# Optimization experiments

Hardware: AMD Instinct MI355X
Metric: run time of the kernel (lower is better)

## Reference

```python
import jax, jax.numpy as jnp
import numpy as np

# static sizes (see shape_source)
IN_SIZE = 50000
M = 3            # n_modalities
N0 = 40960       # layer-0 sampled source nodes
N1 = 16384       # layer-0 dst == layer-1 src
B = 4096         # batch (final dst nodes)
HEADS = 4
DIM = 64
HD = HEADS * DIM # 256, integration_size
DEG0, DEG1 = 16, 16
E0, E1 = N1 * DEG0, B * DEG1
NEG_SLOPE = 0.2  # GATConv default negative_slope


def gat_conv(x_src, e_src, e_dst, n_dst, W, att, bias):
    """PyG GATConv with bipartite input (x, None): attention uses only alpha_l.
    x_src: [Ns, HD]; W: [HD, HD]; att: [1, H, C]; returns [n_dst, HD]."""
    x_l = (x_src @ W.T).reshape(-1, HEADS, DIM)            # [Ns, H, C]
    alpha_l = (x_l * att).sum(-1)                          # [Ns, H]
    logits = jax.nn.leaky_relu(alpha_l[e_src], NEG_SLOPE)  # [E, H]
    m = jax.ops.segment_max(logits, e_dst, num_segments=n_dst)
    m = jnp.where(jnp.isfinite(m), m, 0.0)                 # guard empty segments
    e = jnp.exp(logits - m[e_dst])
    denom = jax.ops.segment_sum(e, e_dst, num_segments=n_dst)
    a = e / (denom[e_dst] + 1e-16)                         # edge softmax per dst
    msg = x_l[e_src] * a[:, :, None]                       # [E, H, C]
    out = jax.ops.segment_sum(msg, e_dst, num_segments=n_dst)
    return out.reshape(n_dst, HD) + bias


def interp(scales_param, mask, key):
    """Interp module, evaluate=False, idxs = range(M)."""
    scales = jax.nn.softmax(scales_param, axis=-1)         # [1, M]
    rm = jax.random.randint(key, mask.shape, 0, 2).astype(jnp.float32)
    rm = rm + (1.0 / (1.0 + rm.sum(-1)) ** 20)[:, None]
    rm = rm + (1.0 / (mask.sum(-1) ** 20))[:, None]
    rm = jax.lax.stop_gradient(jnp.floor(rm))              # .int().float()
    rm = rm / (rm + 1e-10)
    m = mask * rm
    m = jax.nn.softmax(m + (1.0 - m) * (-1e10), axis=-1)   # [B, M]
    return scales, m


def setup_inputs() -> dict:
    key = jax.random.key(0)
    ks = jax.random.split(key, 12)
    s = 0.05
    return {
        "masks": jnp.ones((B, M), jnp.float32),
        "n_ids": jax.random.randint(ks[0], (M, N0), 0, IN_SIZE, dtype=jnp.int32),
        "e0_src": jax.random.randint(ks[1], (M, E0), 0, N0, dtype=jnp.int32),
        "e0_dst": jnp.repeat(jnp.arange(N1, dtype=jnp.int32), DEG0),
        "e1_src": jax.random.randint(ks[2], (M, E1), 0, N1, dtype=jnp.int32),
        "e1_dst": jnp.repeat(jnp.arange(B, dtype=jnp.int32), DEG1),
        "pre_W": jax.random.normal(ks[3], (M, HD, IN_SIZE), jnp.float32) * s,
        "pre_b": jax.random.normal(ks[4], (M, HD), jnp.float32) * s,
        "gat_W": jax.random.normal(ks[5], (M, HD, HD), jnp.float32) * s,
        "gat_att": jax.random.normal(ks[6], (M, 1, HEADS, DIM), jnp.float32) * s,
        "gat_b": jax.random.normal(ks[7], (M, HD), jnp.float32) * s,
        "scales_param": jnp.full((1, M), 1.0 / M, jnp.float32),
        "emb_W": jax.random.normal(ks[8], (128, HD), jnp.float32) * s,
        "emb_b": jax.random.normal(ks[9], (128,), jnp.float32) * s,
    }


def reference(masks, n_ids, e0_src, e0_dst, e1_src, e1_dst,
              pre_W, pre_b, gat_W, gat_att, gat_b,
              scales_param, emb_W, emb_b):
    scales, interp_masks = interp(scales_param, masks, jax.random.key(42))
    x_mod = jnp.zeros((B, HD), dtype=masks.dtype)
    for i in range(M):  # small fixed modality loop (structurally distinct params)
        # one-hot(n_id) @ W.T + b  ==  gather of columns of W (same math)
        x = jnp.take(pre_W[i], n_ids[i], axis=1).T + pre_b[i]        # [N0, HD]
        g0 = gat_conv(x, e0_src[i], e0_dst, N1, gat_W[i], gat_att[i], gat_b[i])
        g1 = gat_conv(g0, e1_src[i], e1_dst, B, gat_W[i], gat_att[i], gat_b[i])
        # x_store_layer = [g0[:B] (sliced), g0[:B] (x_pre), g1]; x = sum + g1
        xm = 2.0 * g0[:B] + 2.0 * g1                                  # [B, HD]
        xm = scales[:, i] * interp_masks[:, i].reshape(-1, 1) * xm
        x_mod = x_mod + xm
    emb = x_mod @ emb_W.T + emb_b                                     # [B, 128]
    dot = emb @ emb.T                                                 # [B, B]
    return dot, emb, scales
```

## Files before the change

kernel.cpp:

```cpp
#include <hip/hip_runtime.h>
#include <hip/hip_bf16.h>
#include <cstdint>

#define IN_SZ 50000
#define NM 3
#define N0 40960
#define N1 16384
#define NB 4096
#define HD 256
#define DEG 16
#define E0 (N1*DEG)
#define E1 (NB*DEG)

using short8v = __attribute__((ext_vector_type(8))) short;
using floatx4 = __attribute__((ext_vector_type(4))) float;
typedef unsigned short ushort_t;

__device__ __forceinline__ ushort_t f2bf(float f){
  uint32_t u = __float_as_uint(f);
  uint32_t r = u + 0x7FFFu + ((u>>16)&1u);
  return (ushort_t)(r>>16);
}
__device__ __forceinline__ float bf2f(ushort_t h){
  return __uint_as_float(((uint32_t)h)<<16);
}
__device__ __forceinline__ void gload_lds16(const ushort_t* g, ushort_t* l){
  __builtin_amdgcn_global_load_lds(
      (const __attribute__((address_space(1))) void*)g,
      (__attribute__((address_space(3))) void*)l, 16, 0, 0);
}

__device__ __forceinline__ uint32_t rotl32(uint32_t x, uint32_t d){ return (x<<d)|(x>>(32u-d)); }

__device__ void tf2x32(uint32_t k0, uint32_t k1, uint32_t c0, uint32_t c1,
                       uint32_t& y0, uint32_t& y1)
{
  uint32_t ks2 = k0 ^ k1 ^ 0x1BD11BDAu;
  uint32_t x0 = c0 + k0, x1 = c1 + k1;
#define R4(a,b,c,d) \
  x0+=x1; x1=rotl32(x1,a); x1^=x0; \
  x0+=x1; x1=rotl32(x1,b); x1^=x0; \
  x0+=x1; x1=rotl32(x1,c); x1^=x0; \
  x0+=x1; x1=rotl32(x1,d); x1^=x0;
  R4(13,15,26,6)  x0+=k1;  x1+=ks2+1u;
  R4(17,29,16,24) x0+=ks2; x1+=k0+2u;
  R4(13,15,26,6)  x0+=k0;  x1+=k1+3u;
  R4(17,29,16,24) x0+=k1;  x1+=ks2+4u;
  R4(13,15,26,6)  x0+=ks2; x1+=k0+5u;
#undef R4
  y0=x0; y1=x1;
}

__global__ void interp_coef_k(const float* __restrict__ masks, const float* __restrict__ sp,
                              float* __restrict__ coef, float* __restrict__ scales_out)
{
  int b = blockIdx.x*256 + threadIdx.x;
  if (b >= NB) return;
  float s0=sp[0], s1=sp[1], s2=sp[2];
  float mx = fmaxf(s0,fmaxf(s1,s2));
  float e0=expf(s0-mx), e1=expf(s1-mx), e2=expf(s2-mx);
  float inv = 1.f/(e0+e1+e2);
  float sc[3] = {e0*inv, e1*inv, e2*inv};
  if (b == 0){ scales_out[0]=sc[0]; scales_out[1]=sc[1]; scales_out[2]=sc[2]; }

  uint32_t bits[3];
  uint32_t K0,K1, t0,t1;
  tf2x32(0u,42u,0u,1u,K0,K1);
  for (int i=0;i<3;i++){
    uint32_t idx = (uint32_t)(b*3+i);
    tf2x32(K0,K1,0u,idx,t0,t1);
    bits[i] = (t0 ^ t1) & 1u;
  }
  float mk[3] = {masks[b*3+0], masks[b*3+1], masks[b*3+2]};
  float msum = mk[0]+mk[1]+mk[2];
  float rs = (float)(bits[0]+bits[1]+bits[2]);
  float add = powf(1.f/(1.f+rs), 20.f) + powf(1.f/msum, 20.f);
  float lg[3]; float lmax = -1e30f;
  for (int i=0;i<3;i++){
    float rm = floorf((float)bits[i] + add);
    rm = rm/(rm+1e-10f);
    float mm = mk[i]*rm;
    lg[i] = mm + (1.f-mm)*(-1e10f);
    lmax = fmaxf(lmax, lg[i]);
  }
  float es[3], ssum=0.f;
  for (int i=0;i<3;i++){ es[i]=expf(lg[i]-lmax); ssum+=es[i]; }
  for (int i=0;i<3;i++) coef[b*3+i] = sc[i]*es[i]/ssum;
}

__global__ __launch_bounds__(256) void transp_k(const float* __restrict__ Wb,
                                                ushort_t* __restrict__ WT_b)
{
  int i = blockIdx.z;
  const float* W = Wb + (size_t)i*HD*IN_SZ;
  ushort_t* WT = WT_b + (size_t)i*IN_SZ*HD;
  __shared__ float tile[32][33];
  int c0 = blockIdx.x*32, k0 = blockIdx.y*32;
  int tx = threadIdx.x & 31, tg = threadIdx.x >> 5;
#pragma unroll
  for (int j=0;j<4;j++){
    int k = k0 + tg*4 + j, c = c0 + tx;
    tile[tg*4+j][tx] = (c < IN_SZ) ? W[(size_t)k*IN_SZ + c] : 0.f;
  }
  __syncthreads();
#pragma unroll
  for (int j=0;j<4;j++){
    int c = c0 + tg*4 + j, k = k0 + tx;
    if (c < IN_SZ) WT[(size_t)c*HD + k] = f2bf(tile[tx][tg*4+j]);
  }
}

__global__ void split_k(const float* __restrict__ src, ushort_t* __restrict__ hi,
                        ushort_t* __restrict__ lo, int n)
{
  int g = blockIdx.x*256 + threadIdx.x;
  if (g >= n) return;
  float v = src[g];
  ushort_t h = f2bf(v);
  hi[g] = h;
  lo[g] = f2bf(v - bf2f(h));
}

__global__ void bias_gemv_k(const float* __restrict__ pre_b, const float* __restrict__ gat_W,
                            float* __restrict__ bias2)
{
  int i = blockIdx.x, o = threadIdx.x;
  const float* W = gat_W + (size_t)i*HD*HD + (size_t)o*HD;
  const float* b = pre_b + i*HD;
  float s = 0.f;
  for (int k=0;k<HD;k++) s = fmaf(b[k], W[k], s);
  bias2[i*HD + o] = s;
}

template<bool HAS_IDS, bool ADD_BIAS>
__global__ __launch_bounds__(256) void gemm2(
    const ushort_t* __restrict__ A_b, size_t a_stride,
    const int* __restrict__ ids_b, int ids_n,
    const ushort_t* __restrict__ Whi_b, const ushort_t* __restrict__ Wlo_b,
    const float* __restrict__ bias2_b,
    ushort_t* __restrict__ C_b, size_t c_stride,
    const float* __restrict__ att_b, float* __restrict__ alpha_b, size_t al_stride)
{
  int i = blockIdx.z;
  int bn0 = blockIdx.y * 128;
  int brow = blockIdx.x * 128;
  const ushort_t* A = A_b + (size_t)i*a_stride;
  const ushort_t* Whi = Whi_b + (size_t)i*HD*HD;
  const ushort_t* Wlo = Wlo_b + (size_t)i*HD*HD;
  ushort_t* C = C_b + (size_t)i*c_stride;
  const float* att = att_b + (size_t)i*HD;
  float* alpha = alpha_b + (size_t)i*al_stride;

  __shared__ __align__(16) ushort_t smem[2][24*512];
  __shared__ int sid[128];
  int t = threadIdx.x, wave = t>>6, lane = t&63;
  int l15 = lane&15, kq = lane>>4;

  if constexpr (HAS_IDS){
    if (t < 128) sid[t] = ids_b[(size_t)i*ids_n + brow + t];
    __syncthreads();
  }
  int row0, row1;
  if constexpr (HAS_IDS){ row0 = sid[wave*16 + l15]; row1 = sid[(wave+4)*16 + l15]; }
  else                  { row0 = brow + wave*16 + l15; row1 = brow + (wave+4)*16 + l15; }

  const ushort_t* gsrc[6];
  gsrc[0] = A + (size_t)row0*HD + kq*8;
  gsrc[1] = A + (size_t)row1*HD + kq*8;
#pragma unroll
  for (int j=2;j<6;j++){
    int idx = wave + 4*(j-2);
    int ct = idx>>1, h = idx&1;
    const ushort_t* W = h ? Wlo : Whi;
    gsrc[j] = W + (size_t)(bn0 + ct*16 + l15)*HD + kq*8;
  }

  floatx4 acc[4][4];
#pragma unroll
  for (int r=0;r<4;r++)
#pragma unroll
    for (int c=0;c<4;c++) acc[r][c] = (floatx4){0.f,0.f,0.f,0.f};

  int wm = wave>>1, wn = wave&1;

#pragma unroll
  for (int j=0;j<6;j++)
    gload_lds16(gsrc[j], &smem[0][(wave + 4*j)*512]);
  __syncthreads();

  for (int cc=0; cc<8; cc++){
    int buf = cc & 1;
    if (cc < 7){
      int k0 = (cc+1)*32;
#pragma unroll
      for (int j=0;j<6;j++)
        gload_lds16(gsrc[j] + k0, &smem[buf^1][(wave + 4*j)*512]);
    }
    short8v a[4];
#pragma unroll
    for (int r=0;r<4;r++)
      a[r] = *reinterpret_cast<const short8v*>(&smem[buf][(wm*4+r)*512 + lane*8]);
#pragma unroll
    for (int c=0;c<4;c++){
      int ct = wn*4+c;
      short8v bh = *reinterpret_cast<const short8v*>(&smem[buf][(8+ct*2)*512 + lane*8]);
      short8v bl = *reinterpret_cast<const short8v*>(&smem[buf][(9+ct*2)*512 + lane*8]);
#pragma unroll
      for (int r=0;r<4;r++){
        acc[r][c] = __builtin_amdgcn_mfma_f32_16x16x32_bf16(a[r], bh, acc[r][c], 0,0,0);
        acc[r][c] = __builtin_amdgcn_mfma_f32_16x16x32_bf16(a[r], bl, acc[r][c], 0,0,0);
      }
    }
    __syncthreads();
  }

  float attv[4], bias2v[4];
#pragma unroll
  for (int c=0;c<4;c++){
    int col = bn0 + (wn*4+c)*16 + l15;
    attv[c] = att[col];
    if constexpr (ADD_BIAS) bias2v[c] = bias2_b[i*HD + col];
  }
  int head = (bn0>>6) + wn;
#pragma unroll
  for (int r=0;r<4;r++){
    int rowb = brow + wm*64 + r*16 + kq*4;
    if constexpr (ADD_BIAS){
#pragma unroll
      for (int c=0;c<4;c++)
#pragma unroll
        for (int j=0;j<4;j++) acc[r][c][j] += bias2v[c];
    }
#pragma unroll
    for (int j=0;j<4;j++){
      size_t rw = (size_t)(rowb + j)*HD;
#pragma unroll
      for (int c=0;c<4;c++)
        C[rw + bn0 + (wn*4+c)*16 + l15] = f2bf(acc[r][c][j]);
    }
#pragma unroll
    for (int j=0;j<4;j++){
      float p = acc[r][0][j]*attv[0] + acc[r][1][j]*attv[1]
              + acc[r][2][j]*attv[2] + acc[r][3][j]*attv[3];
      p += __shfl_xor(p, 1, 64);
      p += __shfl_xor(p, 2, 64);
      p += __shfl_xor(p, 4, 64);
      p += __shfl_xor(p, 8, 64);
      if (l15 == 0){
        float lg = p > 0.f ? p : 0.2f*p;
        alpha[(size_t)(rowb + j)*4 + head] = lg;
      }
    }
  }
}

__global__ __launch_bounds__(128) void gat_msg0(
    const ushort_t* __restrict__ xlhi_b, const float* __restrict__ alpha_b,
    const int* __restrict__ esrc_b, const float* __restrict__ bias_b,
    uint32_t* __restrict__ g0_u)
{
  int i = blockIdx.y, d = blockIdx.x, t = threadIdx.x;
  const ushort_t* xl = xlhi_b + (size_t)i*N0*HD;
  const float* alpha = alpha_b + (size_t)i*N0*4;
  const float* bias = bias_b + i*HD;
  __shared__ int src[16];
  __shared__ float aw[16][4];
  if (t < 16) src[t] = esrc_b[(size_t)i*E0 + d*16 + t];
  __syncthreads();
  if (t < 64){
    int e = t&15, h = t>>4;
    float l = alpha[(size_t)src[e]*4 + h];
    float m = l;
#pragma unroll
    for (int off=1; off<16; off<<=1) m = fmaxf(m, __shfl_xor(m, off, 64));
    float ex = expf(l - m);
    float s = ex;
#pragma unroll
    for (int off=1; off<16; off<<=1) s += __shfl_xor(s, off, 64);
    aw[e][h] = ex / (s + 1e-16f);
  }
  __syncthreads();
  int h = t >> 5;
  float a0=0.f, a1=0.f;
#pragma unroll
  for (int e=0;e<16;e++){
    uint32_t u = *reinterpret_cast<const uint32_t*>(xl + (size_t)src[e]*HD + 2*t);
    float w = aw[e][h];
    a0 = fmaf(w, bf2f((ushort_t)(u & 0xffffu)), a0);
    a1 = fmaf(w, bf2f((ushort_t)(u >> 16)), a1);
  }
  float v0 = a0 + bias[2*t], v1 = a1 + bias[2*t+1];
  g0_u[((size_t)i*N1 + d)*128 + t] = (uint32_t)f2bf(v0) | ((uint32_t)f2bf(v1)<<16);
}

__global__ __launch_bounds__(128) void gat_msg1(
    const ushort_t* __restrict__ xl1hi, const float* __restrict__ alpha1,
    const int* __restrict__ e1src, const float* __restrict__ gat_b,
    const uint32_t* __restrict__ g0_u, const float* __restrict__ coef,
    float* __restrict__ xmod)
{
  int d = blockIdx.x, t = threadIdx.x;
  __shared__ int src[16];
  __shared__ float aw[16][4];
  float o0 = 0.f, o1 = 0.f;
  for (int i=0;i<NM;i++){
    if (t < 16) src[t] = e1src[(size_t)i*E1 + d*16 + t];
    __syncthreads();
    if (t < 64){
      int e = t&15, h = t>>4;
      float l = alpha1[((size_t)i*N1 + src[e])*4 + h];
      float m = l;
#pragma unroll
      for (int off=1; off<16; off<<=1) m = fmaxf(m, __shfl_xor(m, off, 64));
      float ex = expf(l - m);
      float s = ex;
#pragma unroll
      for (int off=1; off<16; off<<=1) s += __shfl_xor(s, off, 64);
      aw[e][h] = ex / (s + 1e-16f);
    }
    __syncthreads();
    const ushort_t* xl = xl1hi + (size_t)i*N1*HD;
    int h = t >> 5;
    float a0=0.f, a1=0.f;
#pragma unroll
    for (int e=0;e<16;e++){
      uint32_t u = *reinterpret_cast<const uint32_t*>(xl + (size_t)src[e]*HD + 2*t);
      float w = aw[e][h];
      a0 = fmaf(w, bf2f((ushort_t)(u & 0xffffu)), a0);
      a1 = fmaf(w, bf2f((ushort_t)(u >> 16)), a1);
    }
    uint32_t gh = g0_u[((size_t)i*N1 + d)*128 + t];
    float g00 = bf2f((ushort_t)(gh & 0xffffu));
    float g01 = bf2f((ushort_t)(gh >> 16));
    const float* bias = gat_b + i*HD;
    float cv = coef[d*3 + i];
    o0 += cv*(2.f*g00 + 2.f*(a0 + bias[2*t]));
    o1 += cv*(2.f*g01 + 2.f*(a1 + bias[2*t+1]));
    __syncthreads();
  }
  *reinterpret_cast<float2*>(&xmod[(size_t)d*HD + 2*t]) = make_float2(o0, o1);
}

__global__ void transp_embW(const float* __restrict__ w, float* __restrict__ wt)
{
  int g = blockIdx.x*256 + threadIdx.x;
  int j = g >> 8, k = g & 255;
  wt[k*128 + j] = w[g];
}

__global__ __launch_bounds__(256) void emb_gemm(
  const float* __restrict__ xmod, const float* __restrict__ wT,
  const float* __restrict__ eb, float* __restrict__ emb,
  ushort_t* __restrict__ ehi, ushort_t* __restrict__ elo)
{
  __shared__ float xs[32][260];
  int t = threadIdx.x;
  int brow = blockIdx.x * 32;
#pragma unroll
  for (int j=0;j<8;j++){
    int linear = j*256+t;
    int row = linear >> 6;
    int kq = linear & 63;
    float4 f = *reinterpret_cast<const float4*>(&xmod[(size_t)(brow+row)*256 + kq*4]);
    xs[row][kq*4+0]=f.x; xs[row][kq*4+1]=f.y; xs[row][kq*4+2]=f.z; xs[row][kq*4+3]=f.w;
  }
  __syncthreads();
  int tj = t & 127, th = t >> 7;
  float acc[16];
#pragma unroll
  for(int r=0;r<16;r++) acc[r]=0.f;
  for (int k=0;k<256;k++){
    float w = wT[k*128 + tj];
#pragma unroll
    for (int r=0;r<16;r++) acc[r] = fmaf(xs[th*16+r][k], w, acc[r]);
  }
  float bias = eb[tj];
#pragma unroll
  for (int r=0;r<16;r++){
    size_t idx = (size_t)(brow+th*16+r)*128 + tj;
    float v = acc[r] + bias;
    emb[idx] = v;
    ushort_t hb = f2bf(v);
    ehi[idx] = hb;
    elo[idx] = f2bf(v - bf2f(hb));
  }
}

__global__ __launch_bounds__(256) void dot_mfma(
    const ushort_t* __restrict__ Ehi, const ushort_t* __restrict__ Elo,
    float* __restrict__ dot)
{
  __shared__ __align__(16) ushort_t lb[2][16384];
  int t = threadIdx.x, wave = t>>6, lane = t&63;
  int arow0 = blockIdx.y*128, brow0 = blockIdx.x*128;
  {
    const ushort_t* srcp = (t<128) ? Ehi : Elo;
    ushort_t* dstb = lb[(t<128)?0:1];
    int o = t & 127;
    const ushort_t* rp = srcp + (size_t)(brow0+o)*128;
#pragma unroll
    for (int g=0; g<16; g++){
      short8v v = *reinterpret_cast<const short8v*>(rp + g*8);
      int c = g>>2, grp = g&3;
      int lidx = c*4096 + (o>>4)*512 + ((grp<<4)|(o&15))*8;
      *reinterpret_cast<short8v*>(&dstb[lidx]) = v;
    }
  }
  __syncthreads();

  floatx4 acc[2][8];
#pragma unroll
  for (int rt=0;rt<2;rt++)
#pragma unroll
    for (int ot=0;ot<8;ot++) acc[rt][ot] = (floatx4){0.f,0.f,0.f,0.f};

  int ar0 = arow0 + wave*32 + (lane&15);
  int ar1 = ar0 + 16;
  int koff = (lane>>4)*8;
#pragma unroll
  for (int c=0;c<4;c++){
    short8v ah0 = *reinterpret_cast<const short8v*>(Ehi + (size_t)ar0*128 + c*32 + koff);
    short8v ah1 = *reinterpret_cast<const short8v*>(Ehi + (size_t)ar1*128 + c*32 + koff);
    short8v al0 = *reinterpret_cast<const short8v*>(Elo + (size_t)ar0*128 + c*32 + koff);
    short8v al1 = *reinterpret_cast<const short8v*>(Elo + (size_t)ar1*128 + c*32 + koff);
#pragma unroll
    for (int ot=0;ot<8;ot++){
      short8v bh = *reinterpret_cast<const short8v*>(&lb[0][c*4096 + ot*512 + lane*8]);
      short8v bl = *reinterpret_cast<const short8v*>(&lb[1][c*4096 + ot*512 + lane*8]);
      acc[0][ot] = __builtin_amdgcn_mfma_f32_16x16x32_bf16(ah0, bh, acc[0][ot], 0,0,0);
      acc[0][ot] = __builtin_amdgcn_mfma_f32_16x16x32_bf16(ah0, bl, acc[0][ot], 0,0,0);
      acc[0][ot] = __builtin_amdgcn_mfma_f32_16x16x32_bf16(al0, bh, acc[0][ot], 0,0,0);
      acc[1][ot] = __builtin_amdgcn_mfma_f32_16x16x32_bf16(ah1, bh, acc[1][ot], 0,0,0);
      acc[1][ot] = __builtin_amdgcn_mfma_f32_16x16x32_bf16(ah1, bl, acc[1][ot], 0,0,0);
      acc[1][ot] = __builtin_amdgcn_mfma_f32_16x16x32_bf16(al1, bh, acc[1][ot], 0,0,0);
    }
  }
#pragma unroll
  for (int rt=0;rt<2;rt++){
    int rb = arow0 + wave*32 + rt*16 + (lane>>4)*4;
#pragma unroll
    for (int r=0;r<4;r++)
#pragma unroll
      for (int ot=0;ot<8;ot++)
        dot[(size_t)(rb+r)*4096 + brow0 + ot*16 + (lane&15)] = acc[rt][ot][r];
  }
}

extern "C" void kernel_launch(void* const* d_in, const int* in_sizes, int n_in,
                              void* d_out, int out_size, void* d_ws, size_t ws_size,
                              hipStream_t stream) {
  (void)in_sizes; (void)n_in; (void)out_size; (void)ws_size;
  const float* masks   = (const float*)d_in[0];
  const int*   n_ids   = (const int*)d_in[1];
  const int*   e0_src  = (const int*)d_in[2];
  const int*   e1_src  = (const int*)d_in[4];
  const float* pre_W   = (const float*)d_in[6];
  const float* pre_b   = (const float*)d_in[7];
  const float* gat_W   = (const float*)d_in[8];
  const float* gat_att = (const float*)d_in[9];
  const float* gat_b   = (const float*)d_in[10];
  const float* sp      = (const float*)d_in[11];
  const float* emb_W   = (const float*)d_in[12];
  const float* emb_b   = (const float*)d_in[13];

  float* out = (float*)d_out;
  float* dot = out;
  float* emb = out + (size_t)NB*NB;
  float* scales_out = emb + (size_t)NB*128;

  char* p = (char*)d_ws;
  auto alloc = [&](size_t bytes)->char*{ char* r = p; p += (bytes + 255) & ~(size_t)255; return r; };
  ushort_t* WThi  = (ushort_t*)alloc((size_t)NM*IN_SZ*HD*2);
  ushort_t* xlhi  = (ushort_t*)alloc((size_t)NM*N0*HD*2);
  uint32_t* g0u   = (uint32_t*)alloc((size_t)NM*N1*HD*2);
  ushort_t* xl1hi = (ushort_t*)alloc((size_t)NM*N1*HD*2);
  float*    alph0 = (float*)alloc((size_t)NM*N0*4*4);
  float*    alph1 = (float*)alloc((size_t)NM*N1*4*4);
  float*    xmod  = (float*)alloc((size_t)NB*HD*4);
  float*    coef  = (float*)alloc((size_t)NB*3*4);
  float*    wT    = (float*)alloc((size_t)HD*128*4);
  ushort_t* gWhi  = (ushort_t*)alloc((size_t)NM*HD*HD*2);
  ushort_t* gWlo  = (ushort_t*)alloc((size_t)NM*HD*HD*2);
  float*    bias2 = (float*)alloc((size_t)NM*HD*4);
  ushort_t* ehi   = (ushort_t*)alloc((size_t)NB*128*2);
  ushort_t* elo   = (ushort_t*)alloc((size_t)NB*128*2);

  interp_coef_k<<<16, 256, 0, stream>>>(masks, sp, coef, scales_out);
  transp_embW<<<128, 256, 0, stream>>>(emb_W, wT);
  split_k<<<(NM*HD*HD+255)/256, 256, 0, stream>>>(gat_W, gWhi, gWlo, NM*HD*HD);
  bias_gemv_k<<<NM, 256, 0, stream>>>(pre_b, gat_W, bias2);
  transp_k<<<dim3((IN_SZ+31)/32, 8, NM), 256, 0, stream>>>(pre_W, WThi);

  gemm2<true, true><<<dim3(N0/128, 2, NM), 256, 0, stream>>>(
      WThi, (size_t)IN_SZ*HD, n_ids, N0, gWhi, gWlo, bias2,
      xlhi, (size_t)N0*HD, gat_att, alph0, (size_t)N0*4);
  gat_msg0<<<dim3(N1, NM), 128, 0, stream>>>(xlhi, alph0, e0_src, gat_b, g0u);
  gemm2<false, false><<<dim3(N1/128, 2, NM), 256, 0, stream>>>(
      (const ushort_t*)g0u, (size_t)N1*HD, nullptr, 0, gWhi, gWlo, nullptr,
      xl1hi, (size_t)N1*HD, gat_att, alph1, (size_t)N1*4);
  gat_msg1<<<NB, 128, 0, stream>>>(xl1hi, alph1, e1_src, gat_b, g0u, coef, xmod);
  emb_gemm<<<NB/32, 256, 0, stream>>>(xmod, wT, emb_b, emb, ehi, elo);
  dot_mfma<<<dim3(32,32), 256, 0, stream>>>(ehi, elo, dot);
}
```

Before: 291.8 us.

## Precompute GAT projection over full vocabulary and fuse pre_W transpose into GEMM

Rather than transposing pre_W to bf16, gathering rows by n_ids and then multiplying by gat_W, this computes G = pre_W^T · gat_W^T for all IN_SZ rows in one GEMM. That GEMM reads the fp32 pre_W columns directly and converts to bf16 on the fly. gat_msg0 then gathers through n_ids[e_src] into G, and the pre-bias contributions to features and attention logits are folded into small precomputed vectors (bsum, batt). The aim is to remove the separate transpose pass and the intermediate gathered matrix round-trip. In exchange it does more MFMA work (50000 rows instead of 40960) and adds an extra level of indirection in the message kernel.

Result: slower. 317.7 us (+8.9%).

```diff
diff --git a/kernel.cpp b/kernel.cpp
--- a/kernel.cpp
+++ b/kernel.cpp
@@ -88,28 +88,6 @@
   for (int i=0;i<3;i++) coef[b*3+i] = sc[i]*es[i]/ssum;
 }
 
-__global__ __launch_bounds__(256) void transp_k(const float* __restrict__ Wb,
-                                                ushort_t* __restrict__ WT_b)
-{
-  int i = blockIdx.z;
-  const float* W = Wb + (size_t)i*HD*IN_SZ;
-  ushort_t* WT = WT_b + (size_t)i*IN_SZ*HD;
-  __shared__ float tile[32][33];
-  int c0 = blockIdx.x*32, k0 = blockIdx.y*32;
-  int tx = threadIdx.x & 31, tg = threadIdx.x >> 5;
-#pragma unroll
-  for (int j=0;j<4;j++){
-    int k = k0 + tg*4 + j, c = c0 + tx;
-    tile[tg*4+j][tx] = (c < IN_SZ) ? W[(size_t)k*IN_SZ + c] : 0.f;
-  }
-  __syncthreads();
-#pragma unroll
-  for (int j=0;j<4;j++){
-    int c = c0 + tg*4 + j, k = k0 + tx;
-    if (c < IN_SZ) WT[(size_t)c*HD + k] = f2bf(tile[tx][tg*4+j]);
-  }
-}
-
 __global__ void split_k(const float* __restrict__ src, ushort_t* __restrict__ hi,
                         ushort_t* __restrict__ lo, int n)
 {
@@ -121,23 +99,148 @@
   lo[g] = f2bf(v - bf2f(h));
 }
 
-__global__ void bias_gemv_k(const float* __restrict__ pre_b, const float* __restrict__ gat_W,
-                            float* __restrict__ bias2)
+__global__ void bias_prep_k(const float* __restrict__ pre_b, const float* __restrict__ gat_W,
+                            const float* __restrict__ gat_att, const float* __restrict__ gat_b,
+                            float* __restrict__ bsum, float* __restrict__ batt)
 {
   int i = blockIdx.x, o = threadIdx.x;
   const float* W = gat_W + (size_t)i*HD*HD + (size_t)o*HD;
   const float* b = pre_b + i*HD;
   float s = 0.f;
   for (int k=0;k<HD;k++) s = fmaf(b[k], W[k], s);
-  bias2[i*HD + o] = s;
-}
-
-template<bool HAS_IDS, bool ADD_BIAS>
+  bsum[i*HD + o] = s + gat_b[i*HD + o];
+  __shared__ float red[256];
+  red[o] = s * gat_att[i*HD + o];
+  __syncthreads();
+  if (o < 4){
+    float p = 0.f;
+    for (int j=0;j<64;j++) p += red[o*64 + j];
+    batt[i*4 + o] = p;
+  }
+}
+
+__global__ __launch_bounds__(256) void gt_gemm(
+    const float* __restrict__ preW_b,
+    const ushort_t* __restrict__ Whi_b, const ushort_t* __restrict__ Wlo_b,
+    const float* __restrict__ att_b, const float* __restrict__ batt,
+    ushort_t* __restrict__ GT_b, float* __restrict__ alphaG_b)
+{
+  int i = blockIdx.z;
+  int brow = blockIdx.x * 128;
+  const float* pw = preW_b + (size_t)i*HD*IN_SZ;
+  const float* att = att_b + (size_t)i*HD;
+  ushort_t* GT = GT_b + (size_t)i*IN_SZ*HD;
+  float* alphaG = alphaG_b + (size_t)i*IN_SZ*4;
+
+  __shared__ __align__(16) ushort_t As[2][4096];
+  __shared__ __align__(16) ushort_t Bs[2][16384];
+
+  int t = threadIdx.x, wave = t>>6, lane = t&63;
+  int l15 = lane&15, kq = lane>>4;
+
+  const ushort_t* bsrc[8];
+#pragma unroll
+  for (int j=0;j<8;j++){
+    int f = wave + 4*j, ct = f>>1, hs = f&1;
+    const ushort_t* W = (hs ? Wlo_b : Whi_b) + (size_t)i*HD*HD;
+    bsrc[j] = W + (size_t)(ct*16 + l15)*HD + kq*8;
+  }
+  int cl0 = t & 127, q0 = t >> 7;
+  int cl1 = cl0, q1 = q0 + 2;
+  int cg0 = brow + cl0; if (cg0 >= IN_SZ) cg0 = IN_SZ-1;
+  int cg1 = brow + cl1; if (cg1 >= IN_SZ) cg1 = IN_SZ-1;
+  int aoff0 = (cl0>>4)*512 + ((cl0&15) + q0*16)*8;
+  int aoff1 = (cl1>>4)*512 + ((cl1&15) + q1*16)*8;
+
+  floatx4 acc[2][16];
+#pragma unroll
+  for (int r=0;r<2;r++)
+#pragma unroll
+    for (int ct=0;ct<16;ct++) acc[r][ct] = (floatx4){0.f,0.f,0.f,0.f};
+
+  {
+    short8v v0, v1;
+#pragma unroll
+    for (int j=0;j<8;j++){
+      v0[j] = (short)f2bf(pw[(size_t)(q0*8+j)*IN_SZ + cg0]);
+      v1[j] = (short)f2bf(pw[(size_t)(q1*8+j)*IN_SZ + cg1]);
+    }
+    *reinterpret_cast<short8v*>(&As[0][aoff0]) = v0;
+    *reinterpret_cast<short8v*>(&As[0][aoff1]) = v1;
+#pragma unroll
+    for (int j=0;j<8;j++) gload_lds16(bsrc[j], &Bs[0][(wave+4*j)*512]);
+  }
+  __syncthreads();
+
+  for (int cc=0; cc<8; cc++){
+    int buf = cc & 1;
+    float an0[8], an1[8];
+    if (cc < 7){
+      int k0 = (cc+1)*32;
+#pragma unroll
+      for (int j=0;j<8;j++){
+        an0[j] = pw[(size_t)(k0+q0*8+j)*IN_SZ + cg0];
+        an1[j] = pw[(size_t)(k0+q1*8+j)*IN_SZ + cg1];
+      }
+#pragma unroll
+      for (int j=0;j<8;j++) gload_lds16(bsrc[j]+k0, &Bs[buf^1][(wave+4*j)*512]);
+    }
+    short8v a0 = *reinterpret_cast<const short8v*>(&As[buf][(2*wave)*512 + lane*8]);
+    short8v a1 = *reinterpret_cast<const short8v*>(&As[buf][(2*wave+1)*512 + lane*8]);
+#pragma unroll
+    for (int ct=0;ct<16;ct++){
+      short8v bh = *reinterpret_cast<const short8v*>(&Bs[buf][(ct*2)*512 + lane*8]);
+      short8v bl = *reinterpret_cast<const short8v*>(&Bs[buf][(ct*2+1)*512 + lane*8]);
+      acc[0][ct] = __builtin_amdgcn_mfma_f32_16x16x32_bf16(a0, bh, acc[0][ct], 0,0,0);
+      acc[0][ct] = __builtin_amdgcn_mfma_f32_16x16x32_bf16(a0, bl, acc[0][ct], 0,0,0);
+      acc[1][ct] = __builtin_amdgcn_mfma_f32_16x16x32_bf16(a1, bh, acc[1][ct], 0,0,0);
+      acc[1][ct] = __builtin_amdgcn_mfma_f32_16x16x32_bf16(a1, bl, acc[1][ct], 0,0,0);
+    }
+    if (cc < 7){
+      short8v v0, v1;
+#pragma unroll
+      for (int j=0;j<8;j++){ v0[j] = (short)f2bf(an0[j]); v1[j] = (short)f2bf(an1[j]); }
+      *reinterpret_cast<short8v*>(&As[buf^1][aoff0]) = v0;
+      *reinterpret_cast<short8v*>(&As[buf^1][aoff1]) = v1;
+    }
+    __syncthreads();
+  }
+
+  float attv[16];
+#pragma unroll
+  for (int ct=0;ct<16;ct++) attv[ct] = att[ct*16 + l15];
+#pragma unroll
+  for (int r=0;r<2;r++){
+    int rbase = brow + (2*wave+r)*16 + kq*4;
+#pragma unroll
+    for (int j=0;j<4;j++){
+      int c = rbase + j;
+      bool ok = c < IN_SZ;
+      size_t rw = (size_t)c*HD;
+      if (ok){
+#pragma unroll
+        for (int ct=0;ct<16;ct++) GT[rw + ct*16 + l15] = f2bf(acc[r][ct][j]);
+      }
+#pragma unroll
+      for (int h=0;h<4;h++){
+        float p = acc[r][4*h+0][j]*attv[4*h+0] + acc[r][4*h+1][j]*attv[4*h+1]
+                + acc[r][4*h+2][j]*attv[4*h+2] + acc[r][4*h+3][j]*attv[4*h+3];
+        p += __shfl_xor(p, 1, 64);
+        p += __shfl_xor(p, 2, 64);
+        p += __shfl_xor(p, 4, 64);
+        p += __shfl_xor(p, 8, 64);
+        if (l15 == 0 && ok){
+          p += batt[i*4 + h];
+          alphaG[(size_t)c*4 + h] = p > 0.f ? p : 0.2f*p;
+        }
+      }
+    }
+  }
+}
+
 __global__ __launch_bounds__(256) void gemm2(
     const ushort_t* __restrict__ A_b, size_t a_stride,
-    const int* __restrict__ ids_b, int ids_n,
     const ushort_t* __restrict__ Whi_b, const ushort_t* __restrict__ Wlo_b,
-    const float* __restrict__ bias2_b,
     ushort_t* __restrict__ C_b, size_t c_stride,
     const float* __restrict__ att_b, float* __restrict__ alpha_b, size_t al_stride)
 {
@@ -152,17 +255,11 @@
   float* alpha = alpha_b + (size_t)i*al_stride;
 
   __shared__ __align__(16) ushort_t smem[2][24*512];
-  __shared__ int sid[128];
   int t = threadIdx.x, wave = t>>6, lane = t&63;
   int l15 = lane&15, kq = lane>>4;
 
-  if constexpr (HAS_IDS){
-    if (t < 128) sid[t] = ids_b[(size_t)i*ids_n + brow + t];
-    __syncthreads();
-  }
-  int row0, row1;
-  if constexpr (HAS_IDS){ row0 = sid[wave*16 + l15]; row1 = sid[(wave+4)*16 + l15]; }
-  else                  { row0 = brow + wave*16 + l15; row1 = brow + (wave+4)*16 + l15; }
+  int row0 = brow + wave*16 + l15;
+  int row1 = brow + (wave+4)*16 + l15;
 
   const ushort_t* gsrc[6];
   gsrc[0] = A + (size_t)row0*HD + kq*8;
@@ -214,23 +311,13 @@
     __syncthreads();
   }
 
-  float attv[4], bias2v[4];
-#pragma unroll
-  for (int c=0;c<4;c++){
-    int col = bn0 + (wn*4+c)*16 + l15;
-    attv[c] = att[col];
-    if constexpr (ADD_BIAS) bias2v[c] = bias2_b[i*HD + col];
-  }
+  float attv[4];
+#pragma unroll
+  for (int c=0;c<4;c++) attv[c] = att[bn0 + (wn*4+c)*16 + l15];
   int head = (bn0>>6) + wn;
 #pragma unroll
   for (int r=0;r<4;r++){
     int rowb = brow + wm*64 + r*16 + kq*4;
-    if constexpr (ADD_BIAS){
-#pragma unroll
-      for (int c=0;c<4;c++)
-#pragma unroll
-        for (int j=0;j<4;j++) acc[r][c][j] += bias2v[c];
-    }
 #pragma unroll
     for (int j=0;j<4;j++){
       size_t rw = (size_t)(rowb + j)*HD;
@@ -255,21 +342,21 @@
 }
 
 __global__ __launch_bounds__(128) void gat_msg0(
-    const ushort_t* __restrict__ xlhi_b, const float* __restrict__ alpha_b,
-    const int* __restrict__ esrc_b, const float* __restrict__ bias_b,
-    uint32_t* __restrict__ g0_u)
+    const ushort_t* __restrict__ GT_b, const float* __restrict__ alphaG_b,
+    const int* __restrict__ n_ids, const int* __restrict__ esrc_b,
+    const float* __restrict__ bsum_b, uint32_t* __restrict__ g0_u)
 {
   int i = blockIdx.y, d = blockIdx.x, t = threadIdx.x;
-  const ushort_t* xl = xlhi_b + (size_t)i*N0*HD;
-  const float* alpha = alpha_b + (size_t)i*N0*4;
-  const float* bias = bias_b + i*HD;
+  const ushort_t* GT = GT_b + (size_t)i*IN_SZ*HD;
+  const float* alphaG = alphaG_b + (size_t)i*IN_SZ*4;
+  const float* bsum = bsum_b + i*HD;
   __shared__ int src[16];
   __shared__ float aw[16][4];
-  if (t < 16) src[t] = esrc_b[(size_t)i*E0 + d*16 + t];
+  if (t < 16) src[t] = n_ids[(size_t)i*N0 + esrc_b[(size_t)i*E0 + d*16 + t]];
   __syncthreads();
   if (t < 64){
     int e = t&15, h = t>>4;
-    float l = alpha[(size_t)src[e]*4 + h];
+    float l = alphaG[(size_t)src[e]*4 + h];
     float m = l;
 #pragma unroll
     for (int off=1; off<16; off<<=1) m = fmaxf(m, __shfl_xor(m, off, 64));
@@ -284,12 +371,12 @@
   float a0=0.f, a1=0.f;
 #pragma unroll
   for (int e=0;e<16;e++){
-    uint32_t u = *reinterpret_cast<const uint32_t*>(xl + (size_t)src[e]*HD + 2*t);
+    uint32_t u = *reinterpret_cast<const uint32_t*>(GT + (size_t)src[e]*HD + 2*t);
     float w = aw[e][h];
     a0 = fmaf(w, bf2f((ushort_t)(u & 0xffffu)), a0);
     a1 = fmaf(w, bf2f((ushort_t)(u >> 16)), a1);
   }
-  float v0 = a0 + bias[2*t], v1 = a1 + bias[2*t+1];
+  float v0 = a0 + bsum[2*t], v1 = a1 + bsum[2*t+1];
   g0_u[((size_t)i*N1 + d)*128 + t] = (uint32_t)f2bf(v0) | ((uint32_t)f2bf(v1)<<16);
 }
 
@@ -470,33 +557,31 @@
 
   char* p = (char*)d_ws;
   auto alloc = [&](size_t bytes)->char*{ char* r = p; p += (bytes + 255) & ~(size_t)255; return r; };
-  ushort_t* WThi  = (ushort_t*)alloc((size_t)NM*IN_SZ*HD*2);
-  ushort_t* xlhi  = (ushort_t*)alloc((size_t)NM*N0*HD*2);
+  ushort_t* GT    = (ushort_t*)alloc((size_t)NM*IN_SZ*HD*2);
+  float*    alphG = (float*)alloc((size_t)NM*IN_SZ*4*4);
   uint32_t* g0u   = (uint32_t*)alloc((size_t)NM*N1*HD*2);
   ushort_t* xl1hi = (ushort_t*)alloc((size_t)NM*N1*HD*2);
-  float*    alph0 = (float*)alloc((size_t)NM*N0*4*4);
   float*    alph1 = (float*)alloc((size_t)NM*N1*4*4);
   float*    xmod  = (float*)alloc((size_t)NB*HD*4);
   float*    coef  = (float*)alloc((size_t)NB*3*4);
   float*    wT    = (float*)alloc((size_t)HD*128*4);
   ushort_t* gWhi  = (ushort_t*)alloc((size_t)NM*HD*HD*2);
   ushort_t* gWlo  = (ushort_t*)alloc((size_t)NM*HD*HD*2);
-  float*    bias2 = (float*)alloc((size_t)NM*HD*4);
+  float*    bsum  = (float*)alloc((size_t)NM*HD*4);
+  float*    batt  = (float*)alloc((size_t)NM*4*4);
   ushort_t* ehi   = (ushort_t*)alloc((size_t)NB*128*2);
   ushort_t* elo   = (ushort_t*)alloc((size_t)NB*128*2);
 
   interp_coef_k<<<16, 256, 0, stream>>>(masks, sp, coef, scales_out);
   transp_embW<<<128, 256, 0, stream>>>(emb_W, wT);
   split_k<<<(NM*HD*HD+255)/256, 256, 0, stream>>>(gat_W, gWhi, gWlo, NM*HD*HD);
-  bias_gemv_k<<<NM, 256, 0, stream>>>(pre_b, gat_W, bias2);
-  transp_k<<<dim3((IN_SZ+31)/32, 8, NM), 256, 0, stream>>>(pre_W, WThi);
-
-  gemm2<true, true><<<dim3(N0/128, 2, NM), 256, 0, stream>>>(
-      WThi, (size_t)IN_SZ*HD, n_ids, N0, gWhi, gWlo, bias2,
-      xlhi, (size_t)N0*HD, gat_att, alph0, (size_t)N0*4);
-  gat_msg0<<<dim3(N1, NM), 128, 0, stream>>>(xlhi, alph0, e0_src, gat_b, g0u);
-  gemm2<false, false><<<dim3(N1/128, 2, NM), 256, 0, stream>>>(
-      (const ushort_t*)g0u, (size_t)N1*HD, nullptr, 0, gWhi, gWlo, nullptr,
+  bias_prep_k<<<NM, 256, 0, stream>>>(pre_b, gat_W, gat_att, gat_b, bsum, batt);
+
+  gt_gemm<<<dim3((IN_SZ+127)/128, 1, NM), 256, 0, stream>>>(
+      pre_W, gWhi, gWlo, gat_att, batt, GT, alphG);
+  gat_msg0<<<dim3(N1, NM), 128, 0, stream>>>(GT, alphG, n_ids, e0_src, bsum, g0u);
+  gemm2<<<dim3(N1/128, 2, NM), 256, 0, stream>>>(
+      (const ushort_t*)g0u, (size_t)N1*HD, gWhi, gWlo,
       xl1hi, (size_t)N1*HD, gat_att, alph1, (size_t)N1*4);
   gat_msg1<<<NB, 128, 0, stream>>>(xl1hi, alph1, e1_src, gat_b, g0u, coef, xmod);
   emb_gemm<<<NB/32, 256, 0, stream>>>(xmod, wT, emb_b, emb, ehi, elo);
```

## Project full pre_W vocabulary before gathering and fold biases into post-aggregation terms

Applied to the files above, without the earlier changes.

The layer-0 GEMM now projects every padded vocabulary row of the transposed pre_W, with no n_ids gather on the A operand. The gather by n_ids moves into gat_msg0, which becomes a double indirection through n_ids and e0_src. The pre_b projection is pulled out of the GEMM: its attention contribution is a per-head constant added to the logits, and its feature contribution is merged with gat_b and added after softmax aggregation. The transpose kernel also switches to float4 loads and packed bf16 stores. The trade is more GEMM rows and a larger projected buffer (50048 rows instead of 40960) in exchange for contiguous A loads and cheaper bias handling.

Measured after the change: 305.8 us. 1.05x slower.

```diff
diff --git a/kernel.cpp b/kernel.cpp
--- a/kernel.cpp
+++ b/kernel.cpp
@@ -3,6 +3,7 @@
 #include <cstdint>
 
 #define IN_SZ 50000
+#define PADC  50048
 #define NM 3
 #define N0 40960
 #define N1 16384
@@ -88,28 +89,6 @@
   for (int i=0;i<3;i++) coef[b*3+i] = sc[i]*es[i]/ssum;
 }
 
-__global__ __launch_bounds__(256) void transp_k(const float* __restrict__ Wb,
-                                                ushort_t* __restrict__ WT_b)
-{
-  int i = blockIdx.z;
-  const float* W = Wb + (size_t)i*HD*IN_SZ;
-  ushort_t* WT = WT_b + (size_t)i*IN_SZ*HD;
-  __shared__ float tile[32][33];
-  int c0 = blockIdx.x*32, k0 = blockIdx.y*32;
-  int tx = threadIdx.x & 31, tg = threadIdx.x >> 5;
-#pragma unroll
-  for (int j=0;j<4;j++){
-    int k = k0 + tg*4 + j, c = c0 + tx;
-    tile[tg*4+j][tx] = (c < IN_SZ) ? W[(size_t)k*IN_SZ + c] : 0.f;
-  }
-  __syncthreads();
-#pragma unroll
-  for (int j=0;j<4;j++){
-    int c = c0 + tg*4 + j, k = k0 + tx;
-    if (c < IN_SZ) WT[(size_t)c*HD + k] = f2bf(tile[tx][tg*4+j]);
-  }
-}
-
 __global__ void split_k(const float* __restrict__ src, ushort_t* __restrict__ hi,
                         ushort_t* __restrict__ lo, int n)
 {
@@ -121,25 +100,62 @@
   lo[g] = f2bf(v - bf2f(h));
 }
 
-__global__ void bias_gemv_k(const float* __restrict__ pre_b, const float* __restrict__ gat_W,
-                            float* __restrict__ bias2)
+__global__ void bias_prep_k(const float* __restrict__ pre_b, const float* __restrict__ gat_W,
+                            const float* __restrict__ gat_att, const float* __restrict__ gat_b,
+                            float* __restrict__ bsum, float* __restrict__ batt)
 {
   int i = blockIdx.x, o = threadIdx.x;
   const float* W = gat_W + (size_t)i*HD*HD + (size_t)o*HD;
   const float* b = pre_b + i*HD;
   float s = 0.f;
   for (int k=0;k<HD;k++) s = fmaf(b[k], W[k], s);
-  bias2[i*HD + o] = s;
-}
-
-template<bool HAS_IDS, bool ADD_BIAS>
+  bsum[i*HD + o] = s + gat_b[i*HD + o];
+  __shared__ float red[256];
+  red[o] = s * gat_att[i*HD + o];
+  __syncthreads();
+  if (o < 4){
+    float p = 0.f;
+    for (int j=0;j<64;j++) p += red[o*64 + j];
+    batt[i*4 + o] = p;
+  }
+}
+
+__global__ __launch_bounds__(256) void transp4_k(const float* __restrict__ Wb,
+                                                 ushort_t* __restrict__ WT_b)
+{
+  int i = blockIdx.z;
+  const float* W = Wb + (size_t)i*HD*IN_SZ;
+  ushort_t* WT = WT_b + (size_t)i*(size_t)PADC*HD;
+  __shared__ float tile[32][33];
+  int c0 = blockIdx.x*32, k0 = blockIdx.y*32;
+  int t = threadIdx.x;
+  int lk = t>>3, lq = t&7;
+  int cbase = c0 + lq*4;
+  float4 f;
+  if (cbase + 3 < IN_SZ){
+    f = *reinterpret_cast<const float4*>(&W[(size_t)(k0+lk)*IN_SZ + cbase]);
+  } else {
+    float tmp[4] = {0.f,0.f,0.f,0.f};
+#pragma unroll
+    for (int e=0;e<4;e++) if (cbase+e < IN_SZ) tmp[e] = W[(size_t)(k0+lk)*IN_SZ + cbase+e];
+    f = make_float4(tmp[0],tmp[1],tmp[2],tmp[3]);
+  }
+  tile[lk][lq*4+0]=f.x; tile[lk][lq*4+1]=f.y; tile[lk][lq*4+2]=f.z; tile[lk][lq*4+3]=f.w;
+  __syncthreads();
+  int sc = t>>3, skq = t&7;
+  uint32_t lo = (uint32_t)f2bf(tile[skq*4+0][sc]) | ((uint32_t)f2bf(tile[skq*4+1][sc])<<16);
+  uint32_t hi = (uint32_t)f2bf(tile[skq*4+2][sc]) | ((uint32_t)f2bf(tile[skq*4+3][sc])<<16);
+  uint2 pack = make_uint2(lo, hi);
+  *reinterpret_cast<uint2*>(&WT[(size_t)(c0+sc)*HD + k0 + skq*4]) = pack;
+}
+
+template<bool GTMODE>
 __global__ __launch_bounds__(256) void gemm2(
     const ushort_t* __restrict__ A_b, size_t a_stride,
-    const int* __restrict__ ids_b, int ids_n,
     const ushort_t* __restrict__ Whi_b, const ushort_t* __restrict__ Wlo_b,
-    const float* __restrict__ bias2_b,
     ushort_t* __restrict__ C_b, size_t c_stride,
-    const float* __restrict__ att_b, float* __restrict__ alpha_b, size_t al_stride)
+    const float* __restrict__ att_b, float* __restrict__ alpha_b, size_t al_stride,
+    const float* __restrict__ batt, int m_valid)
 {
   int i = blockIdx.z;
   int bn0 = blockIdx.y * 128;
@@ -152,17 +168,11 @@
   float* alpha = alpha_b + (size_t)i*al_stride;
 
   __shared__ __align__(16) ushort_t smem[2][24*512];
-  __shared__ int sid[128];
   int t = threadIdx.x, wave = t>>6, lane = t&63;
   int l15 = lane&15, kq = lane>>4;
 
-  if constexpr (HAS_IDS){
-    if (t < 128) sid[t] = ids_b[(size_t)i*ids_n + brow + t];
-    __syncthreads();
-  }
-  int row0, row1;
-  if constexpr (HAS_IDS){ row0 = sid[wave*16 + l15]; row1 = sid[(wave+4)*16 + l15]; }
-  else                  { row0 = brow + wave*16 + l15; row1 = brow + (wave+4)*16 + l15; }
+  int row0 = brow + wave*16 + l15;
+  int row1 = brow + (wave+4)*16 + l15;
 
   const ushort_t* gsrc[6];
   gsrc[0] = A + (size_t)row0*HD + kq*8;
@@ -214,25 +224,18 @@
     __syncthreads();
   }
 
-  float attv[4], bias2v[4];
-#pragma unroll
-  for (int c=0;c<4;c++){
-    int col = bn0 + (wn*4+c)*16 + l15;
-    attv[c] = att[col];
-    if constexpr (ADD_BIAS) bias2v[c] = bias2_b[i*HD + col];
-  }
+  float attv[4];
+#pragma unroll
+  for (int c=0;c<4;c++) attv[c] = att[bn0 + (wn*4+c)*16 + l15];
   int head = (bn0>>6) + wn;
+  float battv = 0.f;
+  if constexpr (GTMODE) battv = batt[i*4 + head];
 #pragma unroll
   for (int r=0;r<4;r++){
     int rowb = brow + wm*64 + r*16 + kq*4;
-    if constexpr (ADD_BIAS){
-#pragma unroll
-      for (int c=0;c<4;c++)
-#pragma unroll
-        for (int j=0;j<4;j++) acc[r][c][j] += bias2v[c];
-    }
 #pragma unroll
     for (int j=0;j<4;j++){
+      if (GTMODE && rowb + j >= m_valid) continue;
       size_t rw = (size_t)(rowb + j)*HD;
 #pragma unroll
       for (int c=0;c<4;c++)
@@ -246,7 +249,8 @@
       p += __shfl_xor(p, 2, 64);
       p += __shfl_xor(p, 4, 64);
       p += __shfl_xor(p, 8, 64);
-      if (l15 == 0){
+      if (l15 == 0 && (!GTMODE || rowb + j < m_valid)){
+        p += battv;
         float lg = p > 0.f ? p : 0.2f*p;
         alpha[(size_t)(rowb + j)*4 + head] = lg;
       }
@@ -255,21 +259,21 @@
 }
 
 __global__ __launch_bounds__(128) void gat_msg0(
-    const ushort_t* __restrict__ xlhi_b, const float* __restrict__ alpha_b,
-    const int* __restrict__ esrc_b, const float* __restrict__ bias_b,
-    uint32_t* __restrict__ g0_u)
+    const ushort_t* __restrict__ GT_b, const float* __restrict__ alphaG_b,
+    const int* __restrict__ n_ids, const int* __restrict__ esrc_b,
+    const float* __restrict__ bsum_b, uint32_t* __restrict__ g0_u)
 {
   int i = blockIdx.y, d = blockIdx.x, t = threadIdx.x;
-  const ushort_t* xl = xlhi_b + (size_t)i*N0*HD;
-  const float* alpha = alpha_b + (size_t)i*N0*4;
-  const float* bias = bias_b + i*HD;
+  const ushort_t* GT = GT_b + (size_t)i*(size_t)PADC*HD;
+  const float* alphaG = alphaG_b + (size_t)i*IN_SZ*4;
+  const float* bsum = bsum_b + i*HD;
   __shared__ int src[16];
   __shared__ float aw[16][4];
-  if (t < 16) src[t] = esrc_b[(size_t)i*E0 + d*16 + t];
+  if (t < 16) src[t] = n_ids[(size_t)i*N0 + esrc_b[(size_t)i*E0 + d*16 + t]];
   __syncthreads();
   if (t < 64){
     int e = t&15, h = t>>4;
-    float l = alpha[(size_t)src[e]*4 + h];
+    float l = alphaG[(size_t)src[e]*4 + h];
     float m = l;
 #pragma unroll
     for (int off=1; off<16; off<<=1) m = fmaxf(m, __shfl_xor(m, off, 64));
@@ -284,12 +288,12 @@
   float a0=0.f, a1=0.f;
 #pragma unroll
   for (int e=0;e<16;e++){
-    uint32_t u = *reinterpret_cast<const uint32_t*>(xl + (size_t)src[e]*HD + 2*t);
+    uint32_t u = *reinterpret_cast<const uint32_t*>(GT + (size_t)src[e]*HD + 2*t);
     float w = aw[e][h];
     a0 = fmaf(w, bf2f((ushort_t)(u & 0xffffu)), a0);
     a1 = fmaf(w, bf2f((ushort_t)(u >> 16)), a1);
   }
-  float v0 = a0 + bias[2*t], v1 = a1 + bias[2*t+1];
+  float v0 = a0 + bsum[2*t], v1 = a1 + bsum[2*t+1];
   g0_u[((size_t)i*N1 + d)*128 + t] = (uint32_t)f2bf(v0) | ((uint32_t)f2bf(v1)<<16);
 }
 
@@ -470,34 +474,35 @@
 
   char* p = (char*)d_ws;
   auto alloc = [&](size_t bytes)->char*{ char* r = p; p += (bytes + 255) & ~(size_t)255; return r; };
-  ushort_t* WThi  = (ushort_t*)alloc((size_t)NM*IN_SZ*HD*2);
-  ushort_t* xlhi  = (ushort_t*)alloc((size_t)NM*N0*HD*2);
+  ushort_t* WT    = (ushort_t*)alloc((size_t)NM*PADC*HD*2);
+  ushort_t* GT    = (ushort_t*)alloc((size_t)NM*PADC*HD*2);
+  float*    alphG = (float*)alloc((size_t)NM*IN_SZ*4*4);
   uint32_t* g0u   = (uint32_t*)alloc((size_t)NM*N1*HD*2);
   ushort_t* xl1hi = (ushort_t*)alloc((size_t)NM*N1*HD*2);
-  float*    alph0 = (float*)alloc((size_t)NM*N0*4*4);
   float*    alph1 = (float*)alloc((size_t)NM*N1*4*4);
   float*    xmod  = (float*)alloc((size_t)NB*HD*4);
   float*    coef  = (float*)alloc((size_t)NB*3*4);
   float*    wT    = (float*)alloc((size_t)HD*128*4);
   ushort_t* gWhi  = (ushort_t*)alloc((size_t)NM*HD*HD*2);
   ushort_t* gWlo  = (ushort_t*)alloc((size_t)NM*HD*HD*2);
-  float*    bias2 = (float*)alloc((size_t)NM*HD*4);
+  float*    bsum  = (float*)alloc((size_t)NM*HD*4);
+  float*    batt  = (float*)alloc((size_t)NM*4*4);
   ushort_t* ehi   = (ushort_t*)alloc((size_t)NB*128*2);
   ushort_t* elo   = (ushort_t*)alloc((size_t)NB*128*2);
 
   interp_coef_k<<<16, 256, 0, stream>>>(masks, sp, coef, scales_out);
   transp_embW<<<128, 256, 0, stream>>>(emb_W, wT);
   split_k<<<(NM*HD*HD+255)/256, 256, 0, stream>>>(gat_W, gWhi, gWlo, NM*HD*HD);
-  bias_gemv_k<<<NM, 256, 0, stream>>>(pre_b, gat_W, bias2);
-  transp_k<<<dim3((IN_SZ+31)/32, 8, NM), 256, 0, stream>>>(pre_W, WThi);
-
-  gemm2<true, true><<<dim3(N0/128, 2, NM), 256, 0, stream>>>(
-      WThi, (size_t)IN_SZ*HD, n_ids, N0, gWhi, gWlo, bias2,
-      xlhi, (size_t)N0*HD, gat_att, alph0, (size_t)N0*4);
-  gat_msg0<<<dim3(N1, NM), 128, 0, stream>>>(xlhi, alph0, e0_src, gat_b, g0u);
-  gemm2<false, false><<<dim3(N1/128, 2, NM), 256, 0, stream>>>(
-      (const ushort_t*)g0u, (size_t)N1*HD, nullptr, 0, gWhi, gWlo, nullptr,
-      xl1hi, (size_t)N1*HD, gat_att, alph1, (size_t)N1*4);
+  bias_prep_k<<<NM, 256, 0, stream>>>(pre_b, gat_W, gat_att, gat_b, bsum, batt);
+  transp4_k<<<dim3(PADC/32, 8, NM), 256, 0, stream>>>(pre_W, WT);
+
+  gemm2<true><<<dim3(PADC/128, 2, NM), 256, 0, stream>>>(
+      WT, (size_t)PADC*HD, gWhi, gWlo,
+      GT, (size_t)PADC*HD, gat_att, alphG, (size_t)IN_SZ*4, batt, IN_SZ);
+  gat_msg0<<<dim3(N1, NM), 128, 0, stream>>>(GT, alphG, n_ids, e0_src, bsum, g0u);
+  gemm2<false><<<dim3(N1/128, 2, NM), 256, 0, stream>>>(
+      (const ushort_t*)g0u, (size_t)N1*HD, gWhi, gWlo,
+      xl1hi, (size_t)N1*HD, gat_att, alph1, (size_t)N1*4, nullptr, N1);
   gat_msg1<<<NB, 128, 0, stream>>>(xl1hi, alph1, e1_src, gat_b, g0u, coef, xmod);
   emb_gemm<<<NB/32, 256, 0, stream>>>(xmod, wT, emb_b, emb, ehi, elo);
   dot_mfma<<<dim3(32,32), 256, 0, stream>>>(ehi, elo, dot);
```
